# Kernel tuning notes

Hardware: AMD Instinct MI355X
Metric: run time of the kernel (lower is better)

## Reference

```python
import jax, jax.numpy as jnp
import numpy as np

B, S, H, NH = 4, 2048, 1024, 16
DK = H // NH


def setup_inputs() -> dict:
    key = jax.random.key(0)
    ks = jax.random.split(key, 12)
    sd = 1.0 / np.sqrt(H)
    inp = {
        "query": jax.random.normal(ks[0], (B, S, H), jnp.float32),
        "key_": jax.random.normal(ks[1], (B, S, H), jnp.float32),
        "value": jax.random.normal(ks[2], (B, S, H), jnp.float32),
        "mask": jax.random.randint(ks[3], (B, 1, S, S), 0, 2) == 1,
        "Wq": jax.random.uniform(ks[4], (H, H), jnp.float32, -sd, sd),
        "bq": jnp.zeros((H,), jnp.float32),
        "Wk": jax.random.uniform(ks[5], (H, H), jnp.float32, -sd, sd),
        "bk": jnp.zeros((H,), jnp.float32),
        "Wv": jax.random.uniform(ks[6], (H, H), jnp.float32, -sd, sd),
        "bv": jnp.zeros((H,), jnp.float32),
        "Wo": jax.random.uniform(ks[7], (H, H), jnp.float32, -sd, sd),
        "bo": jnp.zeros((H,), jnp.float32),
    }
    return inp


def reference(query, key_, value, mask, Wq, bq, Wk, bk, Wv, bv, Wo, bo):
    b = query.shape[0]
    # projections; nn.Linear computes x @ W^T + b
    q = (query @ Wq.T + bq).reshape(b, -1, NH, DK).transpose(0, 2, 1, 3)  # [B,NH,S,DK]
    k = (key_ @ Wk.T + bk).reshape(b, -1, NH, DK).transpose(0, 2, 1, 3)
    v = (value @ Wv.T + bv).reshape(b, -1, NH, DK).transpose(0, 2, 1, 3)
    scores = jnp.einsum("bhqd,bhkd->bhqk", q, k) / jnp.sqrt(jnp.float32(DK))
    min_val = jnp.finfo(scores.dtype).min
    scores = jnp.where(mask, min_val, scores)
    attn = jax.nn.softmax(scores, axis=-1)
    attn = jnp.where(mask, 0.0, attn)
    # dropout_rate = 0.0 -> identity
    x = jnp.einsum("bhqk,bhkd->bhqd", attn, v)
    x = x.transpose(0, 2, 1, 3).reshape(b, -1, NH * DK)  # [B,S,H]
    return x @ Wo.T + bo
```

## Files before the change

### kernel.cpp

```cpp
#include <hip/hip_runtime.h>
#include <hip/hip_bf16.h>
#include <stdint.h>

#define B_  4
#define S_  2048
#define H_  1024
#define NH_ 16
#define DK_ 64
#define M_  (B_*S_)

typedef unsigned short u16;
typedef __attribute__((ext_vector_type(8))) short bfrag;
typedef __attribute__((ext_vector_type(4))) float facc;
typedef __attribute__((ext_vector_type(16))) float f32x16;
typedef __attribute__((ext_vector_type(4))) unsigned int u32x4;
typedef __attribute__((ext_vector_type(2))) unsigned int u32x2;

__device__ __forceinline__ u16 f2bf(float f) {
  uint32_t u = __float_as_uint(f);
  return (u16)((u + 0x7fffu + ((u >> 16) & 1u)) >> 16);
}

__device__ __forceinline__ uint32_t cvtpk_bf16(float a, float b) {
  uint32_t r;
  asm("v_cvt_pk_bf16_f32 %0, %1, %2" : "=v"(r) : "v"(a), "v"(b));
  return r;
}

__global__ void cvt3_kernel(const float* __restrict__ a0, const float* __restrict__ a1,
                            const float* __restrict__ a2,
                            u16* __restrict__ o0, u16* __restrict__ o1, u16* __restrict__ o2,
                            int n4) {
  const float* in = blockIdx.y == 0 ? a0 : blockIdx.y == 1 ? a1 : a2;
  u16* out = blockIdx.y == 0 ? o0 : blockIdx.y == 1 ? o1 : o2;
  int i = blockIdx.x * blockDim.x + threadIdx.x;
  int stride = gridDim.x * blockDim.x;
  for (; i < n4; i += stride) {
    float4 v = reinterpret_cast<const float4*>(in)[i];
    ushort4 o;
    o.x = f2bf(v.x); o.y = f2bf(v.y); o.z = f2bf(v.z); o.w = f2bf(v.w);
    reinterpret_cast<ushort4*>(out)[i] = o;
  }
}

__global__ void cvt4_kernel(const float* __restrict__ a0, const float* __restrict__ a1,
                            const float* __restrict__ a2, const float* __restrict__ a3,
                            u16* __restrict__ o0, u16* __restrict__ o1,
                            u16* __restrict__ o2, u16* __restrict__ o3,
                            int n4, float s0) {
  int y = blockIdx.y;
  const float* in = y == 0 ? a0 : y == 1 ? a1 : y == 2 ? a2 : a3;
  u16* out = y == 0 ? o0 : y == 1 ? o1 : y == 2 ? o2 : o3;
  float sc = (y == 0) ? s0 : 1.0f;
  int i = blockIdx.x * blockDim.x + threadIdx.x;
  int stride = gridDim.x * blockDim.x;
  for (; i < n4; i += stride) {
    float4 v = reinterpret_cast<const float4*>(in)[i];
    ushort4 o;
    o.x = f2bf(v.x * sc); o.y = f2bf(v.y * sc);
    o.z = f2bf(v.z * sc); o.w = f2bf(v.w * sc);
    reinterpret_cast<ushort4*>(out)[i] = o;
  }
}

__global__ void pack_mask_kernel(const int* __restrict__ m, uint32_t* __restrict__ out) {
  int od = blockIdx.x * blockDim.x + threadIdx.x;
  int bq = od >> 9;
  int rem = od & 511;
  int c = rem >> 4, t = rem & 15;
  int hl = t >> 3, cc = (t >> 2) & 1, bb = t & 3;
  int4 v = *reinterpret_cast<const int4*>(m + (size_t)bq * 2048 + c*64 + 4*hl + 8*bb + 32*cc);
  uint32_t w = (v.x != 0 ? 1u : 0u) | (v.y != 0 ? 0x100u : 0u) |
               (v.z != 0 ? 0x10000u : 0u) | (v.w != 0 ? 0x1000000u : 0u);
  out[od] = w;
}

#define GLD16(gsrc, ldst) \
  __builtin_amdgcn_global_load_lds((const __attribute__((address_space(1))) void*)(gsrc), \
                                   (__attribute__((address_space(3))) void*)(ldst), 16, 0, 0)

#define GEMM_KLOOP(A_, B_, As_, Bs_) \
  for (int k0 = 0; k0 < K; k0 += 64) { \
    const u16* Ab = (A_) + (size_t)m0 * K + k0; \
    const u16* Bb = (B_) + (size_t)n0 * K + k0; \
    _Pragma("unroll") \
    for (int i = 0; i < 4; i++) { \
      int idx = i*256 + tid; \
      int row = idx >> 3, q = idx & 7; \
      int qs = q ^ (row & 7); \
      char* la = (char*)(As_) + i*4096 + wave*1024; \
      char* lb = (char*)(Bs_) + i*4096 + wave*1024; \
      GLD16(Ab + (size_t)row*K + qs*8, la); \
      GLD16(Bb + (size_t)row*K + qs*8, lb); \
    } \
    __syncthreads(); \
    const int sa = (lo & 7) << 4; \
    _Pragma("unroll") \
    for (int kk = 0; kk < 2; kk++) { \
      bfrag af[4], bfv[4]; \
      _Pragma("unroll") \
      for (int t = 0; t < 4; t++) { \
        af[t]  = *reinterpret_cast<const bfrag*>((char*)(As_) + (wr*64 + t*16 + lo)*128 + ((kk*64 + hi*16) ^ sa)); \
        bfv[t] = *reinterpret_cast<const bfrag*>((char*)(Bs_) + (wc*64 + t*16 + lo)*128 + ((kk*64 + hi*16) ^ sa)); \
      } \
      _Pragma("unroll") \
      for (int mt = 0; mt < 4; mt++) \
        _Pragma("unroll") \
        for (int nt = 0; nt < 4; nt++) \
          acc[mt][nt] = __builtin_amdgcn_mfma_f32_16x16x32_bf16(af[mt], bfv[nt], acc[mt][nt], 0, 0, 0); \
    } \
    __syncthreads(); \
  }

__global__ __launch_bounds__(256) void qkv_gemm(const u16* __restrict__ qa, const u16* __restrict__ ka,
                                                const u16* __restrict__ va,
                                                const u16* __restrict__ Wqb, const u16* __restrict__ Wkb,
                                                const u16* __restrict__ Wvb,
                                                const float* __restrict__ bqp, const float* __restrict__ bkp,
                                                const float* __restrict__ bvp, float qbscale,
                                                u16* __restrict__ qh, u16* __restrict__ kh,
                                                u16* __restrict__ vt) {
  constexpr int K = H_;
  __shared__ __align__(16) u16 SH[2][128*64];
  u16* As = SH[0];
  u16* Bs = SH[1];
  const int tid = threadIdx.x;
  const int lane = tid & 63, wave = tid >> 6;
  const int lo = lane & 15, hi = lane >> 4;
  const int wr = wave >> 1, wc = wave & 1;
  const int wsel = blockIdx.y >> 3;
  const int m0 = blockIdx.x * 128, n0 = (blockIdx.y & 7) * 128;
  const u16* A  = wsel == 0 ? qa : wsel == 1 ? ka : va;
  const u16* Bm = wsel == 0 ? Wqb : wsel == 1 ? Wkb : Wvb;
  const float* bias = wsel == 0 ? bqp : wsel == 1 ? bkp : bvp;
  const float bscale = wsel == 0 ? qbscale : 1.0f;
  facc acc[4][4] = {};

  GEMM_KLOOP(A, Bm, As, Bs)

  if (wsel < 2) {
    u16* o = wsel == 0 ? qh : kh;
    #pragma unroll
    for (int nt = 0; nt < 4; nt++) {
      int n = n0 + wc*64 + nt*16 + lo;
      float bv = bias[n] * bscale;
      int hh = n >> 6, d = n & 63;
      #pragma unroll
      for (int mt = 0; mt < 4; mt++) {
        #pragma unroll
        for (int r = 0; r < 4; r++) {
          int m = m0 + wr*64 + mt*16 + hi*4 + r;
          int bb = m >> 11, s = m & (S_ - 1);
          o[(((size_t)bb*NH_ + hh)*S_ + s)*DK_ + d] = f2bf(acc[mt][nt][r] + bv);
        }
      }
    }
  } else {
    u16* scr = &SH[0][0];
    const int bb2 = m0 >> 11, s0r = m0 & (S_ - 1);
    #pragma unroll
    for (int p = 0; p < 2; p++) {
      __syncthreads();
      if (wc == p) {
        #pragma unroll
        for (int nt = 0; nt < 4; nt++) {
          int d = nt*16 + lo;
          float bv = bias[n0 + p*64 + d];
          #pragma unroll
          for (int mt = 0; mt < 4; mt++) {
            #pragma unroll
            for (int r = 0; r < 4; r++) {
              int s = wr*64 + mt*16 + hi*4 + r;
              *(u16*)((char*)scr + d*256 + ((s*2) ^ ((d & 7) << 4))) = f2bf(acc[mt][nt][r] + bv);
            }
          }
        }
      }
      __syncthreads();
      int hh = (n0 >> 6) + p;
      u16* vbase = vt + ((size_t)bb2*NH_ + hh) * DK_ * S_ + s0r;
      #pragma unroll
      for (int i = 0; i < 4; i++) {
        int idx = i*256 + tid;
        int d = idx >> 4, sc = idx & 15;
        bfrag v = *reinterpret_cast<const bfrag*>((char*)scr + d*256 + ((sc*16) ^ ((d & 7) << 4)));
        *reinterpret_cast<bfrag*>(vbase + (size_t)d*S_ + sc*8) = v;
      }
    }
  }
}

__global__ __launch_bounds__(256) void gemm_out(const u16* __restrict__ A, const u16* __restrict__ Bm,
                                                const float* __restrict__ bias, float* __restrict__ o) {
  constexpr int K = H_, N = H_;
  __shared__ __align__(16) u16 As[128*64];
  __shared__ __align__(16) u16 Bs[128*64];
  const int tid = threadIdx.x;
  const int lane = tid & 63, wave = tid >> 6;
  const int lo = lane & 15, hi = lane >> 4;
  const int wr = wave >> 1, wc = wave & 1;
  const int m0 = blockIdx.x * 128, n0 = blockIdx.y * 128;
  facc acc[4][4] = {};

  GEMM_KLOOP(A, Bm, As, Bs)

  #pragma unroll
  for (int nt = 0; nt < 4; nt++) {
    int n = n0 + wc*64 + nt*16 + lo;
    float bv = bias[n];
    #pragma unroll
    for (int mt = 0; mt < 4; mt++) {
      #pragma unroll
      for (int r = 0; r < 4; r++) {
        int m = m0 + wr*64 + mt*16 + hi*4 + r;
        o[(size_t)m*N + n] = acc[mt][nt][r] + bv;
      }
    }
  }
}

__global__ __launch_bounds__(256, 4) void attn_kernel(const u16* __restrict__ Qh, const u16* __restrict__ Kh,
                                                      const u16* __restrict__ Vt, const uint32_t* __restrict__ mbytes,
                                                      u16* __restrict__ xout) {
  __shared__ __align__(16) u16 Ks[2][64*64];
  __shared__ __align__(16) u16 Vs[2][64*64];
  const int tid = threadIdx.x;
  const int lane = tid & 63, wave = tid >> 6;
  const int l31 = lane & 31, hl = lane >> 5;
  const int gid = blockIdx.x;
  const int bh = (gid & 7) * 8 + (gid >> 7);
  const int qt = (gid >> 3) & 15;
  const int b = bh >> 4, hd = bh & 15;
  const int q0 = qt * 128;
  const size_t bhS = (size_t)bh * S_;
  const int swz = (lane & 7) << 4;

  bfrag qf[4];
  {
    const u16* qrow = Qh + (bhS + q0 + wave*32 + l31) * DK_;
    #pragma unroll
    for (int t = 0; t < 4; t++) qf[t] = *reinterpret_cast<const bfrag*>(qrow + t*16 + hl*8);
  }
  const char* mrowb = (const char*)mbytes + ((size_t)b * S_ + q0 + wave*32 + l31) * 2048 + hl*32;

  const int srow = wave*8 + (lane >> 3);
  const int scol = ((lane & 7) ^ (lane >> 3)) * 16;
  const char* ksrc = (const char*)(Kh + bhS * DK_) + (size_t)srow * 128 + scol;
  const char* vsrc = (const char*)(Vt + (size_t)bh * DK_ * S_) + (size_t)srow * (S_*2) + scol;

#define STAGE(buf, c) { \
    char* kl = (char*)Ks[buf] + wave*1024; \
    char* vl = (char*)Vs[buf] + wave*1024; \
    GLD16(ksrc + (size_t)(c)*8192,          kl); \
    GLD16(ksrc + (size_t)(c)*8192 + 4096,   kl + 4096); \
    GLD16(vsrc + (size_t)(c)*128,           vl); \
    GLD16(vsrc + (size_t)(c)*128 + 131072,  vl + 4096); \
  }

  float l_run = 0.f;
  f32x16 accO[2];
  #pragma unroll
  for (int e = 0; e < 16; e++) { accO[0][e] = 0.f; accO[1][e] = 0.f; }

  STAGE(0, 0);
  u32x4 mA_cur = *reinterpret_cast<const u32x4*>(mrowb);
  u32x4 mB_cur = *reinterpret_cast<const u32x4*>(mrowb + 16);
  __syncthreads();

  for (int c = 0; c < 32; c++) {
    const int cur = c & 1;
    if (c + 1 < 32) STAGE(cur ^ 1, c + 1);

    u32x4 mA = mA_cur, mB = mB_cur;
    if (c + 1 < 32) {
      mA_cur = *reinterpret_cast<const u32x4*>(mrowb + (c + 1)*64);
      mB_cur = *reinterpret_cast<const u32x4*>(mrowb + (c + 1)*64 + 16);
    }

    f32x16 s0, s1;
    #pragma unroll
    for (int r = 0; r < 16; r++) {
      float f0 = (float)((mA[r >> 2] >> ((r & 3) * 8)) & 0xffu);
      float f1 = (float)((mB[r >> 2] >> ((r & 3) * 8)) & 0xffu);
      s0[r] = __builtin_fmaf(f0, -1e36f, -8.0f);
      s1[r] = __builtin_fmaf(f1, -1e36f, -8.0f);
    }

    const char* KsB = (const char*)Ks[cur];
    __builtin_amdgcn_s_setprio(1);
    #pragma unroll
    for (int t = 0; t < 4; t++) {
      bfrag k0 = *reinterpret_cast<const bfrag*>(KsB + l31*128        + ((t*32 + hl*16) ^ swz));
      bfrag k1 = *reinterpret_cast<const bfrag*>(KsB + (32 + l31)*128 + ((t*32 + hl*16) ^ swz));
      s0 = __builtin_amdgcn_mfma_f32_32x32x16_bf16(k0, qf[t], s0, 0, 0, 0);
      s1 = __builtin_amdgcn_mfma_f32_32x32x16_bf16(k1, qf[t], s1, 0, 0, 0);
    }
    __builtin_amdgcn_s_setprio(0);

    #pragma unroll
    for (int r = 0; r < 16; r++) {
      s0[r] = __builtin_amdgcn_exp2f(s0[r]);
      s1[r] = __builtin_amdgcn_exp2f(s1[r]);
    }
    float a8[8];
    #pragma unroll
    for (int r = 0; r < 8; r++) a8[r] = (s0[r] + s0[r+8]) + (s1[r] + s1[r+8]);
    l_run += ((a8[0] + a8[1]) + (a8[2] + a8[3])) + ((a8[4] + a8[5]) + (a8[6] + a8[7]));

    u32x4 pa[4];
    #pragma unroll
    for (int kt = 0; kt < 2; kt++) {
      uint32_t W[8];
      #pragma unroll
      for (int j = 0; j < 8; j++)
        W[j] = kt == 0 ? cvtpk_bf16(s0[2*j], s0[2*j+1]) : cvtpk_bf16(s1[2*j], s1[2*j+1]);
      u32x2 r02 = __builtin_amdgcn_permlane32_swap(W[0], W[2], false, false);
      u32x2 r13 = __builtin_amdgcn_permlane32_swap(W[1], W[3], false, false);
      u32x2 r46 = __builtin_amdgcn_permlane32_swap(W[4], W[6], false, false);
      u32x2 r57 = __builtin_amdgcn_permlane32_swap(W[5], W[7], false, false);
      pa[kt*2    ][0] = r02[0]; pa[kt*2    ][1] = r13[0]; pa[kt*2    ][2] = r02[1]; pa[kt*2    ][3] = r13[1];
      pa[kt*2 + 1][0] = r46[0]; pa[kt*2 + 1][1] = r57[0]; pa[kt*2 + 1][2] = r46[1]; pa[kt*2 + 1][3] = r57[1];
    }

    const char* VsB = (const char*)Vs[cur];
    __builtin_amdgcn_s_setprio(1);
    #pragma unroll
    for (int ks = 0; ks < 4; ks++) {
      bfrag pb = __builtin_bit_cast(bfrag, pa[ks]);
      bfrag v0 = *reinterpret_cast<const bfrag*>(VsB + l31*128        + ((ks*32 + hl*16) ^ swz));
      bfrag v1 = *reinterpret_cast<const bfrag*>(VsB + (32 + l31)*128 + ((ks*32 + hl*16) ^ swz));
      accO[0] = __builtin_amdgcn_mfma_f32_32x32x16_bf16(v0, pb, accO[0], 0, 0, 0);
      accO[1] = __builtin_amdgcn_mfma_f32_32x32x16_bf16(v1, pb, accO[1], 0, 0, 0);
    }
    __builtin_amdgcn_s_setprio(0);
    __syncthreads();
  }
#undef STAGE

  float l_tot = l_run + __shfl_xor(l_run, 32);
  float linv = (l_tot > 0.f) ? (1.f / l_tot) : 0.f;
  u16* Xs = (u16*)Ks;
  {
    char* xb = (char*)Xs + (wave*32 + l31) * 128;
    #pragma unroll
    for (int dt = 0; dt < 2; dt++)
      #pragma unroll
      for (int j = 0; j < 8; j++) {
        uint32_t w = cvtpk_bf16(accO[dt][2*j] * linv, accO[dt][2*j+1] * linv);
        int d = dt*32 + ((2*j) & 3) + 8*((2*j) >> 2) + 4*hl;
        *reinterpret_cast<uint32_t*>(xb + ((d*2) ^ swz)) = w;
      }
  }
  __syncthreads();
  {
    int row = tid >> 1, d0 = (tid & 1) * 32;
    int rsw = (row & 7) << 4;
    u16* orow = xout + ((size_t)b * S_ + q0 + row) * H_ + hd * DK_ + d0;
    #pragma unroll
    for (int i = 0; i < 4; i++) {
      bfrag v = *reinterpret_cast<const bfrag*>((char*)Xs + row*128 + ((d0*2 + i*16) ^ rsw));
      *reinterpret_cast<bfrag*>((char*)orow + i*16) = v;
    }
  }
}

extern "C" void kernel_launch(void* const* d_in, const int* in_sizes, int n_in,
                              void* d_out, int out_size, void* d_ws, size_t ws_size,
                              hipStream_t stream) {
  const float* query = (const float*)d_in[0];
  const float* key_  = (const float*)d_in[1];
  const float* value = (const float*)d_in[2];
  const int*   mask  = (const int*)d_in[3];
  const float* Wq = (const float*)d_in[4];
  const float* bq = (const float*)d_in[5];
  const float* Wk = (const float*)d_in[6];
  const float* bk = (const float*)d_in[7];
  const float* Wv = (const float*)d_in[8];
  const float* bv = (const float*)d_in[9];
  const float* Wo = (const float*)d_in[10];
  const float* bo = (const float*)d_in[11];
  float* out = (float*)d_out;

  char* ws = (char*)d_ws;
  const size_t MB = 1024 * 1024;
  u16* q_act = (u16*)(ws + 0*MB);
  u16* k_act = (u16*)(ws + 16*MB);
  u16* v_act = (u16*)(ws + 32*MB);
  u16* wq_b  = (u16*)(ws + 48*MB);
  u16* wk_b  = (u16*)(ws + 50*MB);
  u16* wv_b  = (u16*)(ws + 52*MB);
  u16* wo_b  = (u16*)(ws + 54*MB);
  u16* qh    = (u16*)(ws + 56*MB);
  u16* kh    = (u16*)(ws + 72*MB);
  u16* vt    = (u16*)(ws + 104*MB);
  u16* xb    = (u16*)(ws + 120*MB);
  uint32_t* mbytes = (uint32_t*)(ws + 136*MB);

  const float QSCALE = 0.125f * 1.44269504088896f;

  const int nact4 = M_ * H_ / 4;
  cvt3_kernel<<<dim3(1024, 3), 256, 0, stream>>>(query, key_, value, q_act, k_act, v_act, nact4);
  const int nw4 = H_ * H_ / 4;
  cvt4_kernel<<<dim3(256, 4), 256, 0, stream>>>(Wq, Wk, Wv, Wo, wq_b, wk_b, wv_b, wo_b, nw4, QSCALE);
  const int ndwords = B_ * S_ * 512;
  pack_mask_kernel<<<ndwords/256, 256, 0, stream>>>(mask, mbytes);

  qkv_gemm<<<dim3(M_/128, 24), 256, 0, stream>>>(q_act, k_act, v_act, wq_b, wk_b, wv_b,
                                                 bq, bk, bv, QSCALE, qh, kh, vt);
  attn_kernel<<<1024, 256, 0, stream>>>(qh, kh, vt, mbytes, xb);
  gemm_out<<<dim3(M_/128, H_/128), 256, 0, stream>>>(xb, wo_b, bo, out);
}
```

Measured before the change: 232.6 us.

## Precompute bf16 mask bias and compute softmax row sums via ones-MFMA

Result: slower. 271.6 us (+16.8%).

```diff
diff --git a/kernel.cpp b/kernel.cpp
--- a/kernel.cpp
+++ b/kernel.cpp
@@ -65,14 +65,16 @@
 
 __global__ void pack_mask_kernel(const int* __restrict__ m, uint32_t* __restrict__ out) {
   int od = blockIdx.x * blockDim.x + threadIdx.x;
-  int bq = od >> 9;
-  int rem = od & 511;
-  int c = rem >> 4, t = rem & 15;
-  int hl = t >> 3, cc = (t >> 2) & 1, bb = t & 3;
-  int4 v = *reinterpret_cast<const int4*>(m + (size_t)bq * 2048 + c*64 + 4*hl + 8*bb + 32*cc);
-  uint32_t w = (v.x != 0 ? 1u : 0u) | (v.y != 0 ? 0x100u : 0u) |
-               (v.z != 0 ? 0x10000u : 0u) | (v.w != 0 ? 0x1000000u : 0u);
-  out[od] = w;
+  int bq = od >> 10;
+  int rem = od & 1023;
+  int c = rem >> 5, t = rem & 31;
+  int hl = t >> 4, cc = (t >> 3) & 1, j = t & 7;
+  int bb = j >> 1, a = (j & 1) * 2;
+  const int* p = m + (size_t)bq * 2048 + c*64 + 32*cc + 4*hl + 8*bb + a;
+  int2 v = *reinterpret_cast<const int2*>(p);
+  uint32_t lo = v.x ? 0xFF80u : 0xC100u;
+  uint32_t hi = v.y ? 0xFF80u : 0xC100u;
+  out[od] = lo | (hi << 16);
 }
 
 #define GLD16(gsrc, ldst) \
@@ -220,7 +222,7 @@
 }
 
 __global__ __launch_bounds__(256, 4) void attn_kernel(const u16* __restrict__ Qh, const u16* __restrict__ Kh,
-                                                      const u16* __restrict__ Vt, const uint32_t* __restrict__ mbytes,
+                                                      const u16* __restrict__ Vt, const uint32_t* __restrict__ mbias,
                                                       u16* __restrict__ xout) {
   __shared__ __align__(16) u16 Ks[2][64*64];
   __shared__ __align__(16) u16 Vs[2][64*64];
@@ -241,7 +243,7 @@
     #pragma unroll
     for (int t = 0; t < 4; t++) qf[t] = *reinterpret_cast<const bfrag*>(qrow + t*16 + hl*8);
   }
-  const char* mrowb = (const char*)mbytes + ((size_t)b * S_ + q0 + wave*32 + l31) * 2048 + hl*32;
+  const char* mrowb = (const char*)mbias + ((size_t)b * S_ + q0 + wave*32 + l31) * 4096 + hl*64;
 
   const int srow = wave*8 + (lane >> 3);
   const int scol = ((lane & 7) ^ (lane >> 3)) * 16;
@@ -257,33 +259,43 @@
     GLD16(vsrc + (size_t)(c)*128 + 131072,  vl + 4096); \
   }
 
-  float l_run = 0.f;
-  f32x16 accO[2];
+  bfrag ones;
   #pragma unroll
-  for (int e = 0; e < 16; e++) { accO[0][e] = 0.f; accO[1][e] = 0.f; }
+  for (int j = 0; j < 8; j++) ones[j] = (short)0x3F80;
+
+  f32x16 accO[2], acc_l;
+  #pragma unroll
+  for (int e = 0; e < 16; e++) { accO[0][e] = 0.f; accO[1][e] = 0.f; acc_l[e] = 0.f; }
 
   STAGE(0, 0);
-  u32x4 mA_cur = *reinterpret_cast<const u32x4*>(mrowb);
-  u32x4 mB_cur = *reinterpret_cast<const u32x4*>(mrowb + 16);
+  u32x4 mA0_c = *reinterpret_cast<const u32x4*>(mrowb);
+  u32x4 mA1_c = *reinterpret_cast<const u32x4*>(mrowb + 16);
+  u32x4 mB0_c = *reinterpret_cast<const u32x4*>(mrowb + 32);
+  u32x4 mB1_c = *reinterpret_cast<const u32x4*>(mrowb + 48);
   __syncthreads();
 
   for (int c = 0; c < 32; c++) {
     const int cur = c & 1;
     if (c + 1 < 32) STAGE(cur ^ 1, c + 1);
 
-    u32x4 mA = mA_cur, mB = mB_cur;
+    u32x4 mA0 = mA0_c, mA1 = mA1_c, mB0 = mB0_c, mB1 = mB1_c;
     if (c + 1 < 32) {
-      mA_cur = *reinterpret_cast<const u32x4*>(mrowb + (c + 1)*64);
-      mB_cur = *reinterpret_cast<const u32x4*>(mrowb + (c + 1)*64 + 16);
+      const char* mn = mrowb + (size_t)(c + 1)*128;
+      mA0_c = *reinterpret_cast<const u32x4*>(mn);
+      mA1_c = *reinterpret_cast<const u32x4*>(mn + 16);
+      mB0_c = *reinterpret_cast<const u32x4*>(mn + 32);
+      mB1_c = *reinterpret_cast<const u32x4*>(mn + 48);
     }
 
     f32x16 s0, s1;
     #pragma unroll
-    for (int r = 0; r < 16; r++) {
-      float f0 = (float)((mA[r >> 2] >> ((r & 3) * 8)) & 0xffu);
-      float f1 = (float)((mB[r >> 2] >> ((r & 3) * 8)) & 0xffu);
-      s0[r] = __builtin_fmaf(f0, -1e36f, -8.0f);
-      s1[r] = __builtin_fmaf(f1, -1e36f, -8.0f);
+    for (int j = 0; j < 8; j++) {
+      uint32_t wA = (j < 4) ? mA0[j] : mA1[j - 4];
+      uint32_t wB = (j < 4) ? mB0[j] : mB1[j - 4];
+      s0[2*j]   = __builtin_bit_cast(float, wA << 16);
+      s0[2*j+1] = __builtin_bit_cast(float, wA & 0xffff0000u);
+      s1[2*j]   = __builtin_bit_cast(float, wB << 16);
+      s1[2*j+1] = __builtin_bit_cast(float, wB & 0xffff0000u);
     }
 
     const char* KsB = (const char*)Ks[cur];
@@ -302,10 +314,6 @@
       s0[r] = __builtin_amdgcn_exp2f(s0[r]);
       s1[r] = __builtin_amdgcn_exp2f(s1[r]);
     }
-    float a8[8];
-    #pragma unroll
-    for (int r = 0; r < 8; r++) a8[r] = (s0[r] + s0[r+8]) + (s1[r] + s1[r+8]);
-    l_run += ((a8[0] + a8[1]) + (a8[2] + a8[3])) + ((a8[4] + a8[5]) + (a8[6] + a8[7]));
 
     u32x4 pa[4];
     #pragma unroll
@@ -331,13 +339,14 @@
       bfrag v1 = *reinterpret_cast<const bfrag*>(VsB + (32 + l31)*128 + ((ks*32 + hl*16) ^ swz));
       accO[0] = __builtin_amdgcn_mfma_f32_32x32x16_bf16(v0, pb, accO[0], 0, 0, 0);
       accO[1] = __builtin_amdgcn_mfma_f32_32x32x16_bf16(v1, pb, accO[1], 0, 0, 0);
+      acc_l   = __builtin_amdgcn_mfma_f32_32x32x16_bf16(ones, pb, acc_l, 0, 0, 0);
     }
     __builtin_amdgcn_s_setprio(0);
     __syncthreads();
   }
 #undef STAGE
 
-  float l_tot = l_run + __shfl_xor(l_run, 32);
+  float l_tot = acc_l[0];
   float linv = (l_tot > 0.f) ? (1.f / l_tot) : 0.f;
   u16* Xs = (u16*)Ks;
   {
@@ -392,9 +401,9 @@
   u16* wo_b  = (u16*)(ws + 54*MB);
   u16* qh    = (u16*)(ws + 56*MB);
   u16* kh    = (u16*)(ws + 72*MB);
-  u16* vt    = (u16*)(ws + 104*MB);
-  u16* xb    = (u16*)(ws + 120*MB);
-  uint32_t* mbytes = (uint32_t*)(ws + 136*MB);
+  u16* vt    = (u16*)(ws + 88*MB);
+  u16* xb    = (u16*)(ws + 104*MB);
+  uint32_t* mbias = (uint32_t*)(ws + 120*MB);
 
   const float QSCALE = 0.125f * 1.44269504088896f;
 
@@ -402,11 +411,11 @@
   cvt3_kernel<<<dim3(1024, 3), 256, 0, stream>>>(query, key_, value, q_act, k_act, v_act, nact4);
   const int nw4 = H_ * H_ / 4;
   cvt4_kernel<<<dim3(256, 4), 256, 0, stream>>>(Wq, Wk, Wv, Wo, wq_b, wk_b, wv_b, wo_b, nw4, QSCALE);
-  const int ndwords = B_ * S_ * 512;
-  pack_mask_kernel<<<ndwords/256, 256, 0, stream>>>(mask, mbytes);
+  const int ndwords = B_ * S_ * 1024;
+  pack_mask_kernel<<<ndwords/256, 256, 0, stream>>>(mask, mbias);
 
   qkv_gemm<<<dim3(M_/128, 24), 256, 0, stream>>>(q_act, k_act, v_act, wq_b, wk_b, wv_b,
                                                  bq, bk, bv, QSCALE, qh, kh, vt);
-  attn_kernel<<<1024, 256, 0, stream>>>(qh, kh, vt, mbytes, xb);
+  attn_kernel<<<1024, 256, 0, stream>>>(qh, kh, vt, mbias, xb);
   gemm_out<<<dim3(M_/128, H_/128), 256, 0, stream>>>(xb, wo_b, bo, out);
 }
```
